# Kernel optimization log

Measured on AMD Instinct MI355X. Metric: run time of the kernel, lower is better.

## Reference

```python
import jax, jax.numpy as jnp
import numpy as np

L, D, H, EXP = 4, 512, 8, 4
HD = D // H
DFF = D * EXP
B, S = 8, 1024
LN_EPS = 1e-3  # keras LayerNormalization default epsilon


def _glorot(key, shape):
    fan_in, fan_out = shape[-2], shape[-1]
    lim = np.sqrt(6.0 / (fan_in + fan_out))
    return jax.random.uniform(key, shape, jnp.float32, -lim, lim)


def setup_inputs() -> dict:
    key = jax.random.key(0)
    ks = jax.random.split(key, 12)
    x = jax.random.normal(ks[0], (B, S, D), jnp.float32)
    # sequence mask from random lengths (mimics tf.sequence_mask(row_lengths))
    lengths = jax.random.randint(ks[1], (B,), S // 2, S + 1)
    mask = (jnp.arange(S)[None, :] < lengths[:, None])  # [B,S] bool
    inp = {
        'x': x, 'mask': mask,
        'Wq': _glorot(ks[2], (L, D, D)),
        'Wk': _glorot(ks[3], (L, D, D)),
        'Wv': _glorot(ks[4], (L, D, D)),
        'Wo': _glorot(ks[5], (L, D, D)),
        'ln1_g': jnp.ones((L, D), jnp.float32),
        'ln1_b': jnp.zeros((L, D), jnp.float32),
        'ln2_g': jnp.ones((L, D), jnp.float32),
        'ln2_b': jnp.zeros((L, D), jnp.float32),
        'W1': _glorot(ks[6], (L, D, DFF)),
        'b1': jnp.zeros((L, DFF), jnp.float32),
        'W2': _glorot(ks[7], (L, DFF, D)),
        'b2': jnp.zeros((L, D), jnp.float32),
    }
    return inp


def _layernorm(x, g, b):
    mu = jnp.mean(x, axis=-1, keepdims=True)
    var = jnp.mean(jnp.square(x - mu), axis=-1, keepdims=True)
    return (x - mu) * jax.lax.rsqrt(var + LN_EPS) * g + b


def _pos_encoding(s, d):
    # matches the source: sin/cos halves with inv freq 10000**(2j/d), j<d/2
    half = d // 2
    p = jnp.arange(s, dtype=jnp.float32)[:, None]          # [S,1]
    inv = 10000.0 ** (2.0 * jnp.arange(half, dtype=jnp.float32) / d)  # [half]
    ang = p / inv[None, :]                                 # [S,half]
    return jnp.concatenate([jnp.sin(ang), jnp.cos(ang)], axis=1)  # [S,D]


def _forward(x, mask, Wq, Wk, Wv, Wo, ln1_g, ln1_b, ln2_g, ln2_b, W1, b1, W2, b2):
    b, s, d = x.shape
    x = x + _pos_encoding(s, d)
    key_mask = mask[:, None, None, :]  # [B,1,1,Sk]
    scale = 1.0 / jnp.sqrt(jnp.float32(HD))
    for l in range(L):
        h = _layernorm(x, ln1_g[l], ln1_b[l])
        q = (h @ Wq[l]).reshape(b, s, H, HD).transpose(0, 2, 1, 3)  # bhsd
        k = (h @ Wk[l]).reshape(b, s, H, HD).transpose(0, 2, 1, 3)
        v = (h @ Wv[l]).reshape(b, s, H, HD).transpose(0, 2, 1, 3)
        scores = jnp.einsum('bhqd,bhkd->bhqk', q, k) * scale
        scores = jnp.where(key_mask, scores, -1e9)
        attn = jax.nn.softmax(scores, axis=-1)
        o = jnp.einsum('bhqk,bhkd->bhqd', attn, v)
        o = o.transpose(0, 2, 1, 3).reshape(b, s, d) @ Wo[l]
        x = x + o  # dropout rate 0 / inference -> identity
        h = _layernorm(x, ln2_g[l], ln2_b[l])
        f = jax.nn.relu(h @ W1[l] + b1[l]) @ W2[l] + b2[l]
        x = x + f
    return x


def reference(x, mask, Wq, Wk, Wv, Wo, ln1_g, ln1_b, ln2_g, ln2_b, W1, b1, W2, b2):
    return _forward(x, mask, Wq, Wk, Wv, Wo, ln1_g, ln1_b, ln2_g, ln2_b, W1, b1, W2, b2)
```

## Files before the change

kernel.cpp:

```cpp
#include <hip/hip_runtime.h>
#include <math.h>

#define NB 8
#define SEQ 1024
#define DM 512
#define NH 8
#define HDIM 64
#define DFF 2048
#define NLAYER 4
#define NTOK (NB * SEQ)
#define QKVD 1536

typedef __attribute__((ext_vector_type(8))) short bf16x8;
typedef __attribute__((ext_vector_type(4))) float f32x4;

__device__ __forceinline__ ushort f2bf(float f) {
    union { float f; unsigned u; } v; v.f = f;
    unsigned r = (v.u + 0x7FFF + ((v.u >> 16) & 1)) >> 16;
    return (ushort)r;
}

__device__ __forceinline__ void async16(const void* g, void* l) {
    __builtin_amdgcn_global_load_lds(
        (const __attribute__((address_space(1))) unsigned int*)g,
        (__attribute__((address_space(3))) unsigned int*)l, 16, 0, 0);
}

__global__ __launch_bounds__(256) void add_pos_kernel(const float* __restrict__ x,
                                                      float* __restrict__ out) {
    int idx4 = blockIdx.x * blockDim.x + threadIdx.x;
    int base = idx4 * 4;
    int d = base & (DM - 1);
    int s = (base >> 9) & (SEQ - 1);
    float4 v = *(const float4*)&x[base];
    float r[4] = {v.x, v.y, v.z, v.w};
#pragma unroll
    for (int i = 0; i < 4; i++) {
        int dd = d + i;
        float pe;
        if (dd < 256) {
            float inv = powf(10000.0f, 2.0f * (float)dd / 512.0f);
            pe = sinf((float)s / inv);
        } else {
            float inv = powf(10000.0f, 2.0f * (float)(dd - 256) / 512.0f);
            pe = cosf((float)s / inv);
        }
        r[i] += pe;
    }
    *(float4*)&out[base] = make_float4(r[0], r[1], r[2], r[3]);
}

__global__ __launch_bounds__(256) void wtrans_kernel(const float* __restrict__ src,
                                                     ushort* __restrict__ dst,
                                                     int K, int N, int rowOff,
                                                     int layerStride) {
    __shared__ float tile[32][36];
    int l = blockIdx.z;
    int kb = blockIdx.y * 32, nb = blockIdx.x * 32;
    const float* s = src + (size_t)l * K * N;
    ushort* d = dst + (size_t)l * layerStride;
    int r = threadIdx.x >> 3, c4 = (threadIdx.x & 7) * 4;
    float4 v = *(const float4*)&s[(size_t)(kb + r) * N + nb + c4];
    *(float4*)&tile[r][c4] = v;
    __syncthreads();
    ushort4 o;
    o.x = f2bf(tile[c4 + 0][r]);
    o.y = f2bf(tile[c4 + 1][r]);
    o.z = f2bf(tile[c4 + 2][r]);
    o.w = f2bf(tile[c4 + 3][r]);
    *(ushort4*)&d[(size_t)(rowOff + nb + r) * K + kb + c4] = o;
}

__global__ __launch_bounds__(256) void vtrans_kernel(const ushort* __restrict__ qkv,
                                                     ushort* __restrict__ vT) {
    __shared__ ushort tile[32][36];
    int b = blockIdx.z;
    int s0 = blockIdx.y * 32, c0 = blockIdx.x * 32;
    int r = threadIdx.x >> 3, q4 = (threadIdx.x & 7) * 4;
    *(ushort4*)&tile[r][q4] =
        *(const ushort4*)&qkv[(size_t)(b * SEQ + s0 + r) * QKVD + 1024 + c0 + q4];
    __syncthreads();
    ushort4 o;
    o.x = tile[q4 + 0][r];
    o.y = tile[q4 + 1][r];
    o.z = tile[q4 + 2][r];
    o.w = tile[q4 + 3][r];
    *(ushort4*)&vT[(size_t)(b * DM + c0 + r) * SEQ + s0 + q4] = o;
}

__global__ __launch_bounds__(256) void ln_kernel(const float* __restrict__ x,
                                                 const float* __restrict__ g,
                                                 const float* __restrict__ bta,
                                                 ushort* __restrict__ out) {
    int w = threadIdx.x >> 6;
    int lane = threadIdx.x & 63;
    size_t row = (size_t)blockIdx.x * 4 + w;
    const float* xr = x + row * DM;
    float4 v0 = *(const float4*)&xr[lane * 4];
    float4 v1 = *(const float4*)&xr[256 + lane * 4];
    float sum = v0.x + v0.y + v0.z + v0.w + v1.x + v1.y + v1.z + v1.w;
#pragma unroll
    for (int off = 32; off > 0; off >>= 1) sum += __shfl_xor(sum, off, 64);
    float mu = sum * (1.0f / 512.0f);
    float d0[8] = {v0.x - mu, v0.y - mu, v0.z - mu, v0.w - mu,
                   v1.x - mu, v1.y - mu, v1.z - mu, v1.w - mu};
    float sq = 0.0f;
#pragma unroll
    for (int i = 0; i < 8; i++) sq = fmaf(d0[i], d0[i], sq);
#pragma unroll
    for (int off = 32; off > 0; off >>= 1) sq += __shfl_xor(sq, off, 64);
    float rs = rsqrtf(sq * (1.0f / 512.0f) + 1e-3f);
    float4 g0 = *(const float4*)&g[lane * 4];
    float4 g1 = *(const float4*)&g[256 + lane * 4];
    float4 b0 = *(const float4*)&bta[lane * 4];
    float4 b1 = *(const float4*)&bta[256 + lane * 4];
    ushort* orow = out + row * DM;
    ushort4 o0, o1;
    o0.x = f2bf(fmaf(d0[0] * rs, g0.x, b0.x));
    o0.y = f2bf(fmaf(d0[1] * rs, g0.y, b0.y));
    o0.z = f2bf(fmaf(d0[2] * rs, g0.z, b0.z));
    o0.w = f2bf(fmaf(d0[3] * rs, g0.w, b0.w));
    o1.x = f2bf(fmaf(d0[4] * rs, g1.x, b1.x));
    o1.y = f2bf(fmaf(d0[5] * rs, g1.y, b1.y));
    o1.z = f2bf(fmaf(d0[6] * rs, g1.z, b1.z));
    o1.w = f2bf(fmaf(d0[7] * rs, g1.w, b1.w));
    *(ushort4*)&orow[lane * 4] = o0;
    *(ushort4*)&orow[256 + lane * 4] = o1;
}

template <int BM, int BN, int KH, int MODE>
__global__ __launch_bounds__(256) void gemm_bf16(const ushort* __restrict__ A,
                                                 const ushort* __restrict__ Bt,
                                                 const float* __restrict__ bias,
                                                 void* __restrict__ Cv,
                                                 int M, int N, int K) {
    static_assert(BM % 64 == 0 && BN % 64 == 0, "tile multiple of 64");
    constexpr int FM = BM / 32;
    constexpr int FN = BN / 32;
    __shared__ __align__(16) ushort As[2][KH * BM * 32];
    __shared__ __align__(16) ushort Bs[2][KH * BN * 32];
    const int tid = threadIdx.x;
    const int lane = tid & 63;
    const int w = tid >> 6;

    const int nx = gridDim.x;
    int wg = blockIdx.y * nx + blockIdx.x;
    int xcd = wg & 7;
    int t = wg >> 3;
    int bx = t % nx;
    int by = (t / nx) * 8 + xcd;
    const int m0 = by * BM, n0 = bx * BN;

    const int wm = (w >> 1) * (BM / 2), wn = (w & 1) * (BN / 2);
    const int fm = lane & 15, fq = lane >> 4;

    f32x4 acc[FM][FN] = {};

    auto stage = [&](int buf, int kt) {
#pragma unroll
        for (int hf = 0; hf < KH; hf++) {
#pragma unroll
            for (int u = 0; u < BM / 64; u++) {
                int chunk = u * 256 + tid;
                int row = chunk >> 2, c = chunk & 3;
                async16(&A[(size_t)(m0 + row) * K + kt + hf * 32 + c * 8],
                        (char*)As[buf] + hf * BM * 64 + chunk * 16);
            }
#pragma unroll
            for (int u = 0; u < BN / 64; u++) {
                int chunk = u * 256 + tid;
                int row = chunk >> 2, c = chunk & 3;
                async16(&Bt[(size_t)(n0 + row) * K + kt + hf * 32 + c * 8],
                        (char*)Bs[buf] + hf * BN * 64 + chunk * 16);
            }
        }
    };

    stage(0, 0);
    __syncthreads();
    int cur = 0;
    for (int kt = 0; kt < K; kt += 32 * KH) {
        if (kt + 32 * KH < K) stage(cur ^ 1, kt + 32 * KH);
#pragma unroll
        for (int hf = 0; hf < KH; hf++) {
            bf16x8 af[FM], bfr[FN];
#pragma unroll
            for (int i = 0; i < FM; i++)
                af[i] = *(const bf16x8*)&As[cur][hf * BM * 32 +
                                                 (wm + i * 16 + fm) * 32 + fq * 8];
#pragma unroll
            for (int j = 0; j < FN; j++)
                bfr[j] = *(const bf16x8*)&Bs[cur][hf * BN * 32 +
                                                  (wn + j * 16 + fm) * 32 + fq * 8];
#pragma unroll
            for (int i = 0; i < FM; i++)
#pragma unroll
                for (int j = 0; j < FN; j++)
                    acc[i][j] = __builtin_amdgcn_mfma_f32_16x16x32_bf16(
                        af[i], bfr[j], acc[i][j], 0, 0, 0);
        }
        __syncthreads();
        cur ^= 1;
    }

#pragma unroll
    for (int i = 0; i < FM; i++) {
#pragma unroll
        for (int j = 0; j < FN; j++) {
            int col = n0 + wn + j * 16 + fm;
#pragma unroll
            for (int r = 0; r < 4; r++) {
                int row = m0 + wm + i * 16 + fq * 4 + r;
                float vv = acc[i][j][r];
                if constexpr (MODE == 0) {
                    ((ushort*)Cv)[(size_t)row * N + col] = f2bf(vv);
                } else if constexpr (MODE == 1) {
                    float* C = (float*)Cv;
                    C[(size_t)row * N + col] += vv;
                } else if constexpr (MODE == 2) {
                    vv += bias[col];
                    vv = fmaxf(vv, 0.0f);
                    ((ushort*)Cv)[(size_t)row * N + col] = f2bf(vv);
                } else {
                    float* C = (float*)Cv;
                    C[(size_t)row * N + col] += vv + bias[col];
                }
            }
        }
    }
}

__global__ __launch_bounds__(256) void attn_mfma(const ushort* __restrict__ QKV,
                                                 const ushort* __restrict__ Vt,
                                                 const int* __restrict__ mask,
                                                 ushort* __restrict__ O) {
    __shared__ __align__(16) ushort Kt[64 * 64];
    __shared__ __align__(16) ushort Vs[64 * 64];
    __shared__ __align__(16) ushort ps[4][16 * 72];
    __shared__ float mskf[64];
    __shared__ int lensh[4];

    const int tid = threadIdx.x, lane = tid & 63, w = tid >> 6;
    const int h = blockIdx.y, b = blockIdx.z;
    const int q0 = blockIdx.x * 64 + w * 16;
    const int fm = lane & 15, fq = lane >> 4;
    ushort* pw = &ps[w][0];
    const float L2E = 1.44269504f;

    int part = mask[b * SEQ + tid] + mask[b * SEQ + 256 + tid] +
               mask[b * SEQ + 512 + tid] + mask[b * SEQ + 768 + tid];
#pragma unroll
    for (int off = 32; off > 0; off >>= 1) part += __shfl_xor(part, off, 64);
    if (lane == 0) lensh[w] = part;

    bf16x8 qf[2];
#pragma unroll
    for (int kk = 0; kk < 2; kk++) {
        bf16x8 t = *(const bf16x8*)&QKV[(size_t)(b * SEQ + q0 + fm) * QKVD + h * HDIM +
                                        kk * 32 + fq * 8];
#pragma unroll
        for (int j = 0; j < 8; j++) {
            union { float f; unsigned u; } vv;
            vv.u = ((unsigned)(ushort)t[j]) << 16;
            vv.f *= 0.125f;
            t[j] = (short)(ushort)(vv.u >> 16);
        }
        qf[kk] = t;
    }

    const int r0 = tid >> 3, c0 = tid & 7;
    const int r1 = r0 + 32;
    const int dk0 = (r0 * 8 + (c0 ^ (r0 & 7))) * 16;
    const int dk1 = (r1 * 8 + (c0 ^ (r1 & 7))) * 16;

    auto gK = [&](int j0, int rr) {
        return (const uint4*)&QKV[(size_t)(b * SEQ + j0 + rr) * QKVD + 512 +
                                  h * HDIM + c0 * 8];
    };
    auto gV = [&](int j0, int rr) {
        return (const uint4*)&Vt[(size_t)((b * NH + h) * HDIM + rr) * SEQ + j0 + c0 * 8];
    };

    uint4 kreg0 = *gK(0, r0), kreg1 = *gK(0, r1);
    uint4 vreg0 = *gV(0, r0), vreg1 = *gV(0, r1);
    int mreg = (tid < 64) ? mask[b * SEQ + tid] : 0;
    *(uint4*)((char*)Kt + dk0) = kreg0;
    *(uint4*)((char*)Kt + dk1) = kreg1;
    *(uint4*)((char*)Vs + dk0) = vreg0;
    *(uint4*)((char*)Vs + dk1) = vreg1;
    if (tid < 64) mskf[tid] = mreg ? 1.0f : 0.0f;
    __syncthreads();

    const int len = lensh[0] + lensh[1] + lensh[2] + lensh[3];
    const int jmax = (len + 63) & ~63;

    f32x4 oacc[4] = {};
    float mrow = -INFINITY, lrow = 0.0f;

    for (int j0 = 0; j0 < jmax; j0 += 64) {
        const bool has_next = (j0 + 64 < jmax);
        if (has_next) {
            kreg0 = *gK(j0 + 64, r0);
            kreg1 = *gK(j0 + 64, r1);
            vreg0 = *gV(j0 + 64, r0);
            vreg1 = *gV(j0 + 64, r1);
            if (tid < 64) mreg = mask[b * SEQ + j0 + 64 + tid];
        }

        f32x4 sc[4] = {};
        __builtin_amdgcn_s_setprio(1);
#pragma unroll
        for (int nt = 0; nt < 4; nt++) {
            int key = nt * 16 + fm;
#pragma unroll
            for (int kk = 0; kk < 2; kk++) {
                bf16x8 kf = *(const bf16x8*)((char*)Kt +
                            (key * 8 + ((kk * 4 + fq) ^ (key & 7))) * 16);
                sc[nt] = __builtin_amdgcn_mfma_f32_16x16x32_bf16(kf, qf[kk], sc[nt], 0, 0, 0);
            }
        }
        __builtin_amdgcn_s_setprio(0);

        float mx = -INFINITY;
#pragma unroll
        for (int nt = 0; nt < 4; nt++)
#pragma unroll
            for (int r = 0; r < 4; r++) mx = fmaxf(mx, sc[nt][r]);
        mx = fmaxf(mx, __shfl_xor(mx, 16));
        mx = fmaxf(mx, __shfl_xor(mx, 32));
        if (!__all(mx - mrow <= 8.0f)) {
            float mn = fmaxf(mrow, mx);
            float alpha = __expf(mrow - mn);
            mrow = mn;
            lrow *= alpha;
#pragma unroll
            for (int nt = 0; nt < 4; nt++)
#pragma unroll
                for (int r = 0; r < 4; r++) oacc[nt][r] *= alpha;
        }

        const float nm2 = -mrow * L2E;
        float sv[4][4];
        float ls = 0.0f;
#pragma unroll
        for (int nt = 0; nt < 4; nt++) {
            f32x4 mv = *(const f32x4*)&mskf[nt * 16 + fq * 4];
#pragma unroll
            for (int r = 0; r < 4; r++) {
                float p = exp2f(fmaf(sc[nt][r], L2E, nm2)) * mv[r];
                sv[nt][r] = p;
                ls += p;
            }
        }
        ls += __shfl_xor(ls, 16);
        ls += __shfl_xor(ls, 32);
        lrow += ls;

#pragma unroll
        for (int nt = 0; nt < 4; nt++) {
            union { float f; unsigned u; } a0, a1, a2, a3;
            a0.f = sv[nt][0]; a1.f = sv[nt][1]; a2.f = sv[nt][2]; a3.f = sv[nt][3];
            unsigned d0 = (a0.u >> 16) | (a1.u & 0xFFFF0000u);
            unsigned d1 = (a2.u >> 16) | (a3.u & 0xFFFF0000u);
            *(uint2*)&pw[fm * 72 + nt * 16 + fq * 4] = make_uint2(d0, d1);
        }

        __builtin_amdgcn_s_setprio(1);
#pragma unroll
        for (int kk = 0; kk < 2; kk++) {
            bf16x8 pf = *(const bf16x8*)&pw[fm * 72 + kk * 32 + fq * 8];
#pragma unroll
            for (int nt = 0; nt < 4; nt++) {
                int dim = nt * 16 + fm;
                bf16x8 vf = *(const bf16x8*)((char*)Vs +
                            (dim * 8 + ((kk * 4 + fq) ^ (dim & 7))) * 16);
                oacc[nt] = __builtin_amdgcn_mfma_f32_16x16x32_bf16(vf, pf, oacc[nt], 0, 0, 0);
            }
        }
        __builtin_amdgcn_s_setprio(0);

        __syncthreads();
        if (has_next) {
            *(uint4*)((char*)Kt + dk0) = kreg0;
            *(uint4*)((char*)Kt + dk1) = kreg1;
            *(uint4*)((char*)Vs + dk0) = vreg0;
            *(uint4*)((char*)Vs + dk1) = vreg1;
            if (tid < 64) mskf[tid] = mreg ? 1.0f : 0.0f;
            __syncthreads();
        }
    }

    float inv = 1.0f / lrow;
#pragma unroll
    for (int nt = 0; nt < 4; nt++) {
        ushort4 o;
        o.x = f2bf(oacc[nt][0] * inv);
        o.y = f2bf(oacc[nt][1] * inv);
        o.z = f2bf(oacc[nt][2] * inv);
        o.w = f2bf(oacc[nt][3] * inv);
        *(ushort4*)&O[(size_t)(b * SEQ + q0 + fm) * DM + h * HDIM + nt * 16 + fq * 4] = o;
    }
}

extern "C" void kernel_launch(void* const* d_in, const int* in_sizes, int n_in,
                              void* d_out, int out_size, void* d_ws, size_t ws_size,
                              hipStream_t stream) {
    const float* x_in = (const float*)d_in[0];
    const int* mask   = (const int*)d_in[1];
    const float* Wq   = (const float*)d_in[2];
    const float* Wk   = (const float*)d_in[3];
    const float* Wv   = (const float*)d_in[4];
    const float* Wo   = (const float*)d_in[5];
    const float* ln1g = (const float*)d_in[6];
    const float* ln1b = (const float*)d_in[7];
    const float* ln2g = (const float*)d_in[8];
    const float* ln2b = (const float*)d_in[9];
    const float* W1   = (const float*)d_in[10];
    const float* b1   = (const float*)d_in[11];
    const float* W2   = (const float*)d_in[12];
    const float* b2   = (const float*)d_in[13];

    float* x = (float*)d_out;
    ushort* wsb = (ushort*)d_ws;
    const size_t U = 1048576;
    ushort* WqkvT = wsb;
    ushort* WoT   = wsb + 3 * U;
    ushort* W1T   = wsb + 4 * U;
    ushort* W2T   = wsb + 8 * U;
    ushort* hb    = wsb + 12 * U;
    ushort* qkv   = wsb + 16 * U;
    ushort* ob    = wsb + 28 * U;
    ushort* vTb   = wsb + 32 * U;
    ushort* f1b   = qkv;

    wtrans_kernel<<<dim3(16, 16, 4), 256, 0, stream>>>(Wq, WqkvT, 512, 512, 0, 786432);
    wtrans_kernel<<<dim3(16, 16, 4), 256, 0, stream>>>(Wk, WqkvT, 512, 512, 512, 786432);
    wtrans_kernel<<<dim3(16, 16, 4), 256, 0, stream>>>(Wv, WqkvT, 512, 512, 1024, 786432);
    wtrans_kernel<<<dim3(16, 16, 4), 256, 0, stream>>>(Wo, WoT, 512, 512, 0, 262144);
    wtrans_kernel<<<dim3(64, 16, 4), 256, 0, stream>>>(W1, W1T, 512, 2048, 0, 1048576);
    wtrans_kernel<<<dim3(16, 64, 4), 256, 0, stream>>>(W2, W2T, 2048, 512, 0, 1048576);

    add_pos_kernel<<<(NTOK * DM / 4) / 256, 256, 0, stream>>>(x_in, x);

    dim3 gQKV(QKVD / 64, NTOK / 128);
    dim3 gProj(DM / 64, NTOK / 64);
    dim3 gFF1(DFF / 64, NTOK / 128);
    dim3 gFF2(DM / 64, NTOK / 64);
    dim3 gAttn(SEQ / 64, NH, NB);
    dim3 gVtr(16, 32, 8);

    for (int l = 0; l < NLAYER; l++) {
        const size_t wOff   = (size_t)l * 262144;
        const size_t wqkvOff= (size_t)l * 786432;
        const size_t w1Off  = (size_t)l * 1048576;

        ln_kernel<<<NTOK / 4, 256, 0, stream>>>(x, ln1g + l * DM, ln1b + l * DM, hb);
        gemm_bf16<128, 64, 1, 0><<<gQKV, 256, 0, stream>>>(hb, WqkvT + wqkvOff, nullptr,
                                                           qkv, NTOK, QKVD, DM);
        vtrans_kernel<<<gVtr, 256, 0, stream>>>(qkv, vTb);
        attn_mfma<<<gAttn, 256, 0, stream>>>(qkv, vTb, mask, ob);
        gemm_bf16<64, 64, 2, 1><<<gProj, 256, 0, stream>>>(ob, WoT + wOff, nullptr, x,
                                                           NTOK, DM, DM);
        ln_kernel<<<NTOK / 4, 256, 0, stream>>>(x, ln2g + l * DM, ln2b + l * DM, hb);
        gemm_bf16<128, 64, 1, 2><<<gFF1, 256, 0, stream>>>(hb, W1T + w1Off,
                                                           b1 + (size_t)l * DFF, f1b,
                                                           NTOK, DFF, DM);
        gemm_bf16<64, 64, 2, 3><<<gFF2, 256, 0, stream>>>(f1b, W2T + w1Off,
                                                          b2 + (size_t)l * DM, x,
                                                          NTOK, DM, DFF);
    }
}
```

Measured before the change: 775.5 us.

## Triple-buffer GEMM LDS staging and skip mask multiply on full attention tiles

Measured after the change: 904.4 us. +16.6%, slower.

```diff
diff --git a/kernel.cpp b/kernel.cpp
--- a/kernel.cpp
+++ b/kernel.cpp
@@ -137,8 +137,9 @@
     static_assert(BM % 64 == 0 && BN % 64 == 0, "tile multiple of 64");
     constexpr int FM = BM / 32;
     constexpr int FN = BN / 32;
-    __shared__ __align__(16) ushort As[2][KH * BM * 32];
-    __shared__ __align__(16) ushort Bs[2][KH * BN * 32];
+    constexpr int OPS = KH * (BM / 64 + BN / 64);
+    __shared__ __align__(16) ushort As[3][KH * BM * 32];
+    __shared__ __align__(16) ushort Bs[3][KH * BN * 32];
     const int tid = threadIdx.x;
     const int lane = tid & 63;
     const int w = tid >> 6;
@@ -146,9 +147,9 @@
     const int nx = gridDim.x;
     int wg = blockIdx.y * nx + blockIdx.x;
     int xcd = wg & 7;
-    int t = wg >> 3;
-    int bx = t % nx;
-    int by = (t / nx) * 8 + xcd;
+    int t0 = wg >> 3;
+    int bx = t0 % nx;
+    int by = (t0 / nx) * 8 + xcd;
     const int m0 = by * BM, n0 = bx * BN;
 
     const int wm = (w >> 1) * (BM / 2), wn = (w & 1) * (BN / 2);
@@ -176,11 +177,14 @@
         }
     };
 
+    const int nsteps = K / (32 * KH);
     stage(0, 0);
-    __syncthreads();
-    int cur = 0;
-    for (int kt = 0; kt < K; kt += 32 * KH) {
-        if (kt + 32 * KH < K) stage(cur ^ 1, kt + 32 * KH);
+    stage(1, 32 * KH);
+    asm volatile("s_waitcnt vmcnt(%0) lgkmcnt(0)\ns_barrier" :: "i"(OPS) : "memory");
+
+    for (int t = 0; t < nsteps; ++t) {
+        const int cur = t % 3;
+        if (t + 2 < nsteps) stage((t + 2) % 3, (t + 2) * 32 * KH);
 #pragma unroll
         for (int hf = 0; hf < KH; hf++) {
             bf16x8 af[FM], bfr[FN];
@@ -199,8 +203,10 @@
                     acc[i][j] = __builtin_amdgcn_mfma_f32_16x16x32_bf16(
                         af[i], bfr[j], acc[i][j], 0, 0, 0);
         }
-        __syncthreads();
-        cur ^= 1;
+        if (t + 2 < nsteps)
+            asm volatile("s_waitcnt vmcnt(%0) lgkmcnt(0)\ns_barrier" :: "i"(OPS) : "memory");
+        else
+            asm volatile("s_waitcnt vmcnt(0) lgkmcnt(0)\ns_barrier" ::: "memory");
     }
 
 #pragma unroll
@@ -340,16 +346,28 @@
         }
 
         const float nm2 = -mrow * L2E;
+        const bool full = (j0 + 64 <= len);
         float sv[4][4];
         float ls = 0.0f;
-#pragma unroll
-        for (int nt = 0; nt < 4; nt++) {
-            f32x4 mv = *(const f32x4*)&mskf[nt * 16 + fq * 4];
-#pragma unroll
-            for (int r = 0; r < 4; r++) {
-                float p = exp2f(fmaf(sc[nt][r], L2E, nm2)) * mv[r];
-                sv[nt][r] = p;
-                ls += p;
+        if (full) {
+#pragma unroll
+            for (int nt = 0; nt < 4; nt++)
+#pragma unroll
+                for (int r = 0; r < 4; r++) {
+                    float p = exp2f(fmaf(sc[nt][r], L2E, nm2));
+                    sv[nt][r] = p;
+                    ls += p;
+                }
+        } else {
+#pragma unroll
+            for (int nt = 0; nt < 4; nt++) {
+                f32x4 mv = *(const f32x4*)&mskf[nt * 16 + fq * 4];
+#pragma unroll
+                for (int r = 0; r < 4; r++) {
+                    float p = exp2f(fmaf(sc[nt][r], L2E, nm2)) * mv[r];
+                    sv[nt][r] = p;
+                    ls += p;
+                }
             }
         }
         ls += __shfl_xor(ls, 16);
```
